# Performance work log

Hardware: AMD Instinct MI355X
Metric: run time of the kernel (lower is better)

## Reference

```python
import jax, jax.numpy as jnp
import numpy as np

B, T = 64, 512
EMBED, HIDDEN, NUM_CLASSES = 512, 1024, 256


def setup_inputs() -> dict:
    key = jax.random.key(0)
    ks = jax.random.split(key, 8)
    x = jax.random.randint(ks[0], (B, T), 0, NUM_CLASSES, dtype=jnp.int32)
    # embedding init uniform(-0.1, 0.1) as in the torch module
    embed = jax.random.uniform(ks[1], (NUM_CLASSES, EMBED), minval=-0.1, maxval=0.1, dtype=jnp.float32)
    s_ih = 1.0 / np.sqrt(HIDDEN)
    W_ih = jax.random.uniform(ks[2], (4 * HIDDEN, EMBED), minval=-s_ih, maxval=s_ih, dtype=jnp.float32)
    W_hh = jax.random.uniform(ks[3], (4 * HIDDEN, HIDDEN), minval=-s_ih, maxval=s_ih, dtype=jnp.float32)
    b_ih = jax.random.uniform(ks[4], (4 * HIDDEN,), minval=-s_ih, maxval=s_ih, dtype=jnp.float32)
    b_hh = jax.random.uniform(ks[5], (4 * HIDDEN,), minval=-s_ih, maxval=s_ih, dtype=jnp.float32)
    s_fc = 1.0 / np.sqrt(HIDDEN)
    fc_W = jax.random.uniform(ks[6], (NUM_CLASSES, HIDDEN), minval=-s_fc, maxval=s_fc, dtype=jnp.float32)
    fc_b = jax.random.uniform(ks[7], (NUM_CLASSES,), minval=-s_fc, maxval=s_fc, dtype=jnp.float32)
    return {"x": x, "embed": embed, "W_ih": W_ih, "W_hh": W_hh,
            "b_ih": b_ih, "b_hh": b_hh, "fc_W": fc_W, "fc_b": fc_b}


def _lstm_forward(x, embed, W_ih, W_hh, b_ih, b_hh, fc_W, fc_b):
    H = W_hh.shape[1]
    x_embed = embed[x]                      # [B, T, E]
    # Precompute input-side gate projections for all timesteps at once.
    gates_x = jnp.einsum('bte,ge->btg', x_embed, W_ih) + (b_ih + b_hh)  # [B, T, 4H]
    gates_x = jnp.transpose(gates_x, (1, 0, 2))  # [T, B, 4H]

    def step(carry, g_x):
        h, c = carry
        gates = g_x + h @ W_hh.T            # [B, 4H]
        i, f, g, o = jnp.split(gates, 4, axis=-1)  # torch gate order: i,f,g,o
        i = jax.nn.sigmoid(i)
        f = jax.nn.sigmoid(f)
        g = jnp.tanh(g)
        o = jax.nn.sigmoid(o)
        c = f * c + i * g
        h = o * jnp.tanh(c)
        return (h, c), h

    Bn = x.shape[0]
    h0 = jnp.zeros((Bn, H), dtype=embed.dtype)
    c0 = jnp.zeros((Bn, H), dtype=embed.dtype)
    _, hs = jax.lax.scan(step, (h0, c0), gates_x)   # hs: [T, B, H]
    hs = jnp.transpose(hs, (1, 0, 2))               # [B, T, H]
    out = jnp.einsum('bth,ch->btc', hs, fc_W) + fc_b  # [B, T, C]
    return out


def reference(x, embed, W_ih, W_hh, b_ih, b_hh, fc_W, fc_b):
    return _lstm_forward(x, embed, W_ih, W_hh, b_ih, b_hh, fc_W, fc_b)
```

## Files before the change

kernel.cpp:

```cpp
#include <hip/hip_runtime.h>
#include <math.h>

#define DEV_INLINE __device__ __forceinline__

static constexpr int Bn = 64;
static constexpr int Tn = 512;
static constexpr int En = 512;
static constexpr int Hn = 1024;
static constexpr int Cn = 256;
static constexpr int Gn = 4 * Hn;

typedef float v4f __attribute__((ext_vector_type(4)));
typedef _Float16 v8h __attribute__((ext_vector_type(8)));

DEV_INLINE float sigmoidf_(float v) { return 1.f / (1.f + __expf(-v)); }

__global__ __launch_bounds__(256) void gemm_tt(
    const float* __restrict__ A, const float* __restrict__ Bm,
    const float* __restrict__ bias1, const float* __restrict__ bias2,
    float* __restrict__ Cm, int M, int N, int K)
{
  constexpr int KC = 32;
  __shared__ float As[KC][68];
  __shared__ float Bs[KC][68];
  const int tid = threadIdx.x;
  const int tx = tid & 15, ty = tid >> 4;
  const int m0 = blockIdx.x * 64, n0 = blockIdx.y * 64;

  float acc[4][4] = {};

  for (int k0 = 0; k0 < K; k0 += KC) {
    __syncthreads();
    #pragma unroll
    for (int j = 0; j < 2; ++j) {
      int f = tid + j * 256;
      int row = f >> 3;
      int c4 = f & 7;
      float4 va = *reinterpret_cast<const float4*>(&A[(size_t)(m0 + row) * K + k0 + c4 * 4]);
      As[c4 * 4 + 0][row] = va.x; As[c4 * 4 + 1][row] = va.y;
      As[c4 * 4 + 2][row] = va.z; As[c4 * 4 + 3][row] = va.w;
      float4 vb = *reinterpret_cast<const float4*>(&Bm[(size_t)(n0 + row) * K + k0 + c4 * 4]);
      Bs[c4 * 4 + 0][row] = vb.x; Bs[c4 * 4 + 1][row] = vb.y;
      Bs[c4 * 4 + 2][row] = vb.z; Bs[c4 * 4 + 3][row] = vb.w;
    }
    __syncthreads();
    #pragma unroll
    for (int k = 0; k < KC; ++k) {
      float4 a4 = *reinterpret_cast<const float4*>(&As[k][ty * 4]);
      float4 b4 = *reinterpret_cast<const float4*>(&Bs[k][tx * 4]);
      float ar[4] = {a4.x, a4.y, a4.z, a4.w};
      float br[4] = {b4.x, b4.y, b4.z, b4.w};
      #pragma unroll
      for (int i = 0; i < 4; ++i)
        #pragma unroll
        for (int j = 0; j < 4; ++j)
          acc[i][j] += ar[i] * br[j];
    }
  }

  #pragma unroll
  for (int j = 0; j < 4; ++j) {
    int n = n0 + tx * 4 + j;
    float bb = bias1[n];
    if (bias2) bb += bias2[n];
    #pragma unroll
    for (int i = 0; i < 4; ++i)
      Cm[(size_t)(m0 + ty * 4 + i) * N + n] = acc[i][j] + bb;
  }
}

__global__ __launch_bounds__(256) void cvt_fcw(
    const float* __restrict__ fcW, _Float16* __restrict__ fcW16)
{
  const int idx = (blockIdx.x * 256 + threadIdx.x) * 8;
  float4 f0 = *(const float4*)(fcW + idx);
  float4 f1 = *(const float4*)(fcW + idx + 4);
  v8h h8;
  h8[0] = (_Float16)f0.x; h8[1] = (_Float16)f0.y;
  h8[2] = (_Float16)f0.z; h8[3] = (_Float16)f0.w;
  h8[4] = (_Float16)f1.x; h8[5] = (_Float16)f1.y;
  h8[6] = (_Float16)f1.z; h8[7] = (_Float16)f1.w;
  *(v8h*)(fcW16 + idx) = h8;
}

__global__ __launch_bounds__(512, 2) void lstm_fused(
    const int* __restrict__ x,
    const float* __restrict__ Whh,
    const float* __restrict__ proj,
    _Float16* __restrict__ hs16,
    int* __restrict__ flags,
    const _Float16* __restrict__ fcW16,
    const float* __restrict__ fcb,
    float* __restrict__ out)
{
  __shared__ __align__(16) char hT[32768];
  __shared__ _Float16 hstage[512];

  const int tid = threadIdx.x;
  const int bid = blockIdx.x;

  const int w = tid >> 6, l = tid & 63;
  const int mrow = l & 15;
  const int kseg = l >> 4;

  const int srcoff = (tid & 15) * 2048 + ((tid >> 4) & 3) * 16 + (tid >> 6) * 64;

  if (bid < 128) {
    const int bg = bid >> 5, hg = bid & 31;
    const int b0 = bg * 16;

    v8h wv[32];
    {
      const float* wr = Whh
        + (size_t)((mrow & 3) * Hn + hg * 32 + w * 4 + (mrow >> 2)) * Hn
        + kseg * 8;
      #pragma unroll
      for (int kk = 0; kk < 32; ++kk) {
        const float* p = wr + kk * 32;
        float4 f0 = *(const float4*)p, f1 = *(const float4*)(p + 4);
        v8h h8;
        h8[0] = (_Float16)f0.x; h8[1] = (_Float16)f0.y;
        h8[2] = (_Float16)f0.z; h8[3] = (_Float16)f0.w;
        h8[4] = (_Float16)f1.x; h8[5] = (_Float16)f1.y;
        h8[6] = (_Float16)f1.z; h8[7] = (_Float16)f1.w;
        wv[kk] = h8;
      }
    }

    const int eb = mrow;
    const int ehc = w * 4 + kseg;
    const int* xp = x + (size_t)(b0 + eb) * Tn;
    float cst = 0.f;

    for (int t = 0; t < Tn; ++t) {
      const int cls = xp[t];
      const float* pb = proj + (size_t)cls * Gn + hg * 32 + ehc;
      float p0 = pb[0], p1 = pb[Hn], p2 = pb[2 * Hn], p3 = pb[3 * Hn];

      if (t > 0) {
        if (tid < 32) {
          const int* fp = flags + ((size_t)(t - 1) * 4 + bg) * 32 + tid;
          int v;
          do {
            asm volatile(
              "global_load_dword %0, %1, off sc0 sc1\n\t"
              "s_waitcnt vmcnt(0)"
              : "=v"(v) : "v"(fp) : "memory");
          } while (v == 0);
        }
        __syncthreads();

        const char* src = (const char*)(hs16 + ((size_t)(t - 1) * Bn + b0) * Hn);
        const char* s0 = src + srcoff;
        v4f r0, r1, r2, r3;
        asm volatile(
          "global_load_dwordx4 %0, %4, off sc0 sc1\n\t"
          "global_load_dwordx4 %1, %5, off sc0 sc1\n\t"
          "global_load_dwordx4 %2, %6, off sc0 sc1\n\t"
          "global_load_dwordx4 %3, %7, off sc0 sc1\n\t"
          "s_waitcnt vmcnt(0)"
          : "=&v"(r0), "=&v"(r1), "=&v"(r2), "=&v"(r3)
          : "v"(s0), "v"(s0 + 512), "v"(s0 + 1024), "v"(s0 + 1536)
          : "memory");
        *(v4f*)(hT + tid * 16 +     0) = r0;
        *(v4f*)(hT + tid * 16 +  8192) = r1;
        *(v4f*)(hT + tid * 16 + 16384) = r2;
        *(v4f*)(hT + tid * 16 + 24576) = r3;
      }
      __syncthreads();

      v4f acc0 = {0.f, 0.f, 0.f, 0.f};
      v4f acc1 = {0.f, 0.f, 0.f, 0.f};
      if (t > 0) {
        #pragma unroll
        for (int kk = 0; kk < 32; kk += 2) {
          v8h a0 = *(const v8h*)(hT + kk * 1024 + l * 16);
          v8h a1 = *(const v8h*)(hT + (kk + 1) * 1024 + l * 16);
          acc0 = __builtin_amdgcn_mfma_f32_16x16x32_f16(wv[kk], a0, acc0, 0, 0, 0);
          acc1 = __builtin_amdgcn_mfma_f32_16x16x32_f16(wv[kk + 1], a1, acc1, 0, 0, 0);
        }
      }

      {
        float g0 = acc0[0] + acc1[0] + p0;
        float g1 = acc0[1] + acc1[1] + p1;
        float g2 = acc0[2] + acc1[2] + p2;
        float g3 = acc0[3] + acc1[3] + p3;
        float ig = sigmoidf_(g0), fg = sigmoidf_(g1);
        float gg = tanhf(g2),     og = sigmoidf_(g3);
        cst = fg * cst + ig * gg;
        hstage[eb * 32 + ehc] = (_Float16)(og * tanhf(cst));
      }
      __syncthreads();

      if (tid < 64) {
        const int b = tid >> 2, part = tid & 3;
        v4f v = *(const v4f*)(hstage + b * 32 + part * 8);
        _Float16* dp = hs16 + ((size_t)t * Bn + b0 + b) * Hn + hg * 32 + part * 8;
        asm volatile(
          "global_store_dwordx4 %0, %1, off sc0 sc1\n\t"
          "s_waitcnt vmcnt(0)"
          :: "v"(dp), "v"(v) : "memory");
        if (tid == 0) {
          int one = 1;
          int* fq = flags + ((size_t)t * 4 + bg) * 32 + hg;
          asm volatile(
            "global_store_dword %0, %1, off sc0 sc1\n\t"
            "s_waitcnt vmcnt(0)"
            :: "v"(fq), "v"(one) : "memory");
        }
      }
    }
  } else {
    const int fid = bid - 128;

    for (int j = 0; j < 16; ++j) {
      const int unit = j * 128 + fid;
      const int t = unit >> 2, bgf = unit & 3;
      const int b0f = bgf * 16;

      if (tid < 32) {
        const int* fp = flags + ((size_t)t * 4 + bgf) * 32 + tid;
        int v;
        for (;;) {
          asm volatile(
            "global_load_dword %0, %1, off sc0 sc1\n\t"
            "s_waitcnt vmcnt(0)"
            : "=v"(v) : "v"(fp) : "memory");
          if (v != 0) break;
          __builtin_amdgcn_s_sleep(16);
        }
      }
      __syncthreads();

      {
        const char* src = (const char*)(hs16 + ((size_t)t * Bn + b0f) * Hn);
        const char* s0 = src + srcoff;
        v4f r0, r1, r2, r3;
        asm volatile(
          "global_load_dwordx4 %0, %4, off sc0 sc1\n\t"
          "global_load_dwordx4 %1, %5, off sc0 sc1\n\t"
          "global_load_dwordx4 %2, %6, off sc0 sc1\n\t"
          "global_load_dwordx4 %3, %7, off sc0 sc1\n\t"
          "s_waitcnt vmcnt(0)"
          : "=&v"(r0), "=&v"(r1), "=&v"(r2), "=&v"(r3)
          : "v"(s0), "v"(s0 + 512), "v"(s0 + 1024), "v"(s0 + 1536)
          : "memory");
        *(v4f*)(hT + tid * 16 +     0) = r0;
        *(v4f*)(hT + tid * 16 +  8192) = r1;
        *(v4f*)(hT + tid * 16 + 16384) = r2;
        *(v4f*)(hT + tid * 16 + 24576) = r3;
      }
      __syncthreads();

      #pragma unroll
      for (int nt = 0; nt < 2; ++nt) {
        const int clsbase = w * 32 + nt * 16;
        v4f acc = {0.f, 0.f, 0.f, 0.f};
        const _Float16* ab = fcW16 + (size_t)(clsbase + mrow) * Hn + kseg * 8;
        #pragma unroll
        for (int kk = 0; kk < 32; ++kk) {
          v8h af = *(const v8h*)(ab + kk * 32);
          v8h bf = *(const v8h*)(hT + kk * 1024 + l * 16);
          acc = __builtin_amdgcn_mfma_f32_16x16x32_f16(af, bf, acc, 0, 0, 0);
        }
        v4f b4 = *(const v4f*)(fcb + clsbase + kseg * 4);
        v4f res = {acc[0] + b4[0], acc[1] + b4[1], acc[2] + b4[2], acc[3] + b4[3]};
        float* op = out + ((size_t)(b0f + mrow) * Tn + t) * Cn + clsbase + kseg * 4;
        *(v4f*)op = res;
      }
    }
  }
}

extern "C" void kernel_launch(void* const* d_in, const int* in_sizes, int n_in,
                              void* d_out, int out_size, void* d_ws, size_t ws_size,
                              hipStream_t stream) {
  const int*   x     = (const int*)  d_in[0];
  const float* embed = (const float*)d_in[1];
  const float* Wih   = (const float*)d_in[2];
  const float* Whh   = (const float*)d_in[3];
  const float* bih   = (const float*)d_in[4];
  const float* bhh   = (const float*)d_in[5];
  const float* fcW   = (const float*)d_in[6];
  const float* fcb   = (const float*)d_in[7];
  float* out = (float*)d_out;

  char* ws = (char*)d_ws;
  const size_t flagBytes = (size_t)Tn * 4 * 32 * 4;
  const size_t projBytes = (size_t)Cn * Gn * sizeof(float);
  const size_t hsBytes   = (size_t)Tn * Bn * Hn * sizeof(_Float16);
  const size_t fw16Bytes = (size_t)Cn * Hn * sizeof(_Float16);
  const size_t need = flagBytes + projBytes + hsBytes + fw16Bytes;
  if (ws_size < need) {
    hipMemsetAsync(d_out, 0, (size_t)out_size * sizeof(float), stream);
    return;
  }
  float*     proj  = (float*)(ws + flagBytes);
  _Float16*  hs16  = (_Float16*)(ws + flagBytes + projBytes);
  _Float16*  fcW16 = (_Float16*)(ws + flagBytes + projBytes + hsBytes);

  hipMemsetAsync(d_ws, 0, flagBytes, stream);

  cvt_fcw<<<128, 256, 0, stream>>>(fcW, fcW16);

  dim3 g1(Cn / 64, Gn / 64);
  gemm_tt<<<g1, 256, 0, stream>>>(embed, Wih, bih, bhh, proj, Cn, Gn, En);

  lstm_fused<<<256, 512, 0, stream>>>(x, Whh, proj, hs16, (int*)d_ws,
                                      fcW16, fcb, out);
}
```

Measured before the change: 1.992 ms.

## Split recurrent step into two half-K phases to overlap flag waits with compute

The recurrent LSTM blocks now wait on the first 16 producer flags, load the first half of h_{t-1}, and run the first half of the MFMA reduction. Meanwhile they wait on the remaining 16 flags and load the second half. This is meant to overlap cross-block synchronisation latency and global loads with matrix work on the serial critical path. The hstage buffer is padded to a stride of 40 to reduce LDS bank conflicts, and the projection-side sleep in the polling loop is lengthened to cut contention. In exchange there are extra __syncthreads per step, including a trailing one.

After: 1.974 ms, median of 2. No clear change (-0.9%).

```diff
diff --git a/kernel.cpp b/kernel.cpp
--- a/kernel.cpp
+++ b/kernel.cpp
@@ -94,7 +94,7 @@
     float* __restrict__ out)
 {
   __shared__ __align__(16) char hT[32768];
-  __shared__ _Float16 hstage[512];
+  __shared__ _Float16 hstage[16 * 40];
 
   const int tid = threadIdx.x;
   const int bid = blockIdx.x;
@@ -137,8 +137,13 @@
       const float* pb = proj + (size_t)cls * Gn + hg * 32 + ehc;
       float p0 = pb[0], p1 = pb[Hn], p2 = pb[2 * Hn], p3 = pb[3 * Hn];
 
+      v4f acc0 = {0.f, 0.f, 0.f, 0.f};
+      v4f acc1 = {0.f, 0.f, 0.f, 0.f};
+
       if (t > 0) {
-        if (tid < 32) {
+        const char* s0 = (const char*)(hs16 + ((size_t)(t - 1) * Bn + b0) * Hn)
+                       + srcoff;
+        if (tid < 16) {
           const int* fp = flags + ((size_t)(t - 1) * 4 + bg) * 32 + tid;
           int v;
           do {
@@ -149,9 +154,108 @@
           } while (v == 0);
         }
         __syncthreads();
-
-        const char* src = (const char*)(hs16 + ((size_t)(t - 1) * Bn + b0) * Hn);
-        const char* s0 = src + srcoff;
+        v4f r0, r1, r2, r3;
+        asm volatile(
+          "global_load_dwordx4 %0, %2, off sc0 sc1\n\t"
+          "global_load_dwordx4 %1, %3, off sc0 sc1"
+          : "=&v"(r0), "=&v"(r1)
+          : "v"(s0), "v"(s0 + 512) : "memory");
+        if (tid >= 16 && tid < 32) {
+          const int* fp = flags + ((size_t)(t - 1) * 4 + bg) * 32 + tid;
+          int v;
+          do {
+            asm volatile(
+              "global_load_dword %0, %1, off sc0 sc1\n\t"
+              "s_waitcnt vmcnt(0)"
+              : "=v"(v) : "v"(fp) : "memory");
+          } while (v == 0);
+        }
+        __syncthreads();
+        asm volatile(
+          "global_load_dwordx4 %0, %2, off sc0 sc1\n\t"
+          "global_load_dwordx4 %1, %3, off sc0 sc1"
+          : "=&v"(r2), "=&v"(r3)
+          : "v"(s0 + 1024), "v"(s0 + 1536) : "memory");
+        asm volatile("s_waitcnt vmcnt(2)" ::: "memory");
+        *(v4f*)(hT + tid * 16 +    0) = r0;
+        *(v4f*)(hT + tid * 16 + 8192) = r1;
+        __syncthreads();
+        #pragma unroll
+        for (int kk = 0; kk < 16; kk += 2) {
+          v8h a0 = *(const v8h*)(hT + kk * 1024 + l * 16);
+          v8h a1 = *(const v8h*)(hT + (kk + 1) * 1024 + l * 16);
+          acc0 = __builtin_amdgcn_mfma_f32_16x16x32_f16(wv[kk], a0, acc0, 0, 0, 0);
+          acc1 = __builtin_amdgcn_mfma_f32_16x16x32_f16(wv[kk + 1], a1, acc1, 0, 0, 0);
+        }
+        asm volatile("s_waitcnt vmcnt(0)" ::: "memory");
+        *(v4f*)(hT + tid * 16 + 16384) = r2;
+        *(v4f*)(hT + tid * 16 + 24576) = r3;
+        __syncthreads();
+        #pragma unroll
+        for (int kk = 16; kk < 32; kk += 2) {
+          v8h a0 = *(const v8h*)(hT + kk * 1024 + l * 16);
+          v8h a1 = *(const v8h*)(hT + (kk + 1) * 1024 + l * 16);
+          acc0 = __builtin_amdgcn_mfma_f32_16x16x32_f16(wv[kk], a0, acc0, 0, 0, 0);
+          acc1 = __builtin_amdgcn_mfma_f32_16x16x32_f16(wv[kk + 1], a1, acc1, 0, 0, 0);
+        }
+      }
+
+      {
+        float g0 = acc0[0] + acc1[0] + p0;
+        float g1 = acc0[1] + acc1[1] + p1;
+        float g2 = acc0[2] + acc1[2] + p2;
+        float g3 = acc0[3] + acc1[3] + p3;
+        float ig = sigmoidf_(g0), fg = sigmoidf_(g1);
+        float gg = tanhf(g2),     og = sigmoidf_(g3);
+        cst = fg * cst + ig * gg;
+        hstage[eb * 40 + ehc] = (_Float16)(og * tanhf(cst));
+      }
+      __syncthreads();
+
+      if (tid < 64) {
+        const int b = tid >> 2, part = tid & 3;
+        v4f v = *(const v4f*)(hstage + b * 40 + part * 8);
+        _Float16* dp = hs16 + ((size_t)t * Bn + b0 + b) * Hn + hg * 32 + part * 8;
+        asm volatile(
+          "global_store_dwordx4 %0, %1, off sc0 sc1\n\t"
+          "s_waitcnt vmcnt(0)"
+          :: "v"(dp), "v"(v) : "memory");
+        if (tid == 0) {
+          int one = 1;
+          int* fq = flags + ((size_t)t * 4 + bg) * 32 + hg;
+          asm volatile(
+            "global_store_dword %0, %1, off sc0 sc1\n\t"
+            "s_waitcnt vmcnt(0)"
+            :: "v"(fq), "v"(one) : "memory");
+        }
+      }
+      __syncthreads();
+    }
+  } else {
+    const int fid = bid - 128;
+
+    for (int j = 0; j < 16; ++j) {
+      const int unit = j * 128 + fid;
+      const int t = unit >> 2, bgf = unit & 3;
+      const int b0f = bgf * 16;
+
+      if (tid < 32) {
+        const int* fp = flags + ((size_t)t * 4 + bgf) * 32 + tid;
+        int v;
+        for (;;) {
+          asm volatile(
+            "global_load_dword %0, %1, off sc0 sc1\n\t"
+            "s_waitcnt vmcnt(0)"
+            : "=v"(v) : "v"(fp) : "memory");
+          if (v != 0) break;
+          __builtin_amdgcn_s_sleep(64);
+        }
+      }
+      __syncthreads();
+
+      {
+        const char* s0 = (const char*)(hs16 + ((size_t)t * Bn + b0f) * Hn)
+                       + srcoff;
         v4f r0, r1, r2, r3;
         asm volatile(
           "global_load_dwordx4 %0, %4, off sc0 sc1\n\t"
@@ -169,90 +273,6 @@
       }
       __syncthreads();
 
-      v4f acc0 = {0.f, 0.f, 0.f, 0.f};
-      v4f acc1 = {0.f, 0.f, 0.f, 0.f};
-      if (t > 0) {
-        #pragma unroll
-        for (int kk = 0; kk < 32; kk += 2) {
-          v8h a0 = *(const v8h*)(hT + kk * 1024 + l * 16);
-          v8h a1 = *(const v8h*)(hT + (kk + 1) * 1024 + l * 16);
-          acc0 = __builtin_amdgcn_mfma_f32_16x16x32_f16(wv[kk], a0, acc0, 0, 0, 0);
-          acc1 = __builtin_amdgcn_mfma_f32_16x16x32_f16(wv[kk + 1], a1, acc1, 0, 0, 0);
-        }
-      }
-
-      {
-        float g0 = acc0[0] + acc1[0] + p0;
-        float g1 = acc0[1] + acc1[1] + p1;
-        float g2 = acc0[2] + acc1[2] + p2;
-        float g3 = acc0[3] + acc1[3] + p3;
-        float ig = sigmoidf_(g0), fg = sigmoidf_(g1);
-        float gg = tanhf(g2),     og = sigmoidf_(g3);
-        cst = fg * cst + ig * gg;
-        hstage[eb * 32 + ehc] = (_Float16)(og * tanhf(cst));
-      }
-      __syncthreads();
-
-      if (tid < 64) {
-        const int b = tid >> 2, part = tid & 3;
-        v4f v = *(const v4f*)(hstage + b * 32 + part * 8);
-        _Float16* dp = hs16 + ((size_t)t * Bn + b0 + b) * Hn + hg * 32 + part * 8;
-        asm volatile(
-          "global_store_dwordx4 %0, %1, off sc0 sc1\n\t"
-          "s_waitcnt vmcnt(0)"
-          :: "v"(dp), "v"(v) : "memory");
-        if (tid == 0) {
-          int one = 1;
-          int* fq = flags + ((size_t)t * 4 + bg) * 32 + hg;
-          asm volatile(
-            "global_store_dword %0, %1, off sc0 sc1\n\t"
-            "s_waitcnt vmcnt(0)"
-            :: "v"(fq), "v"(one) : "memory");
-        }
-      }
-    }
-  } else {
-    const int fid = bid - 128;
-
-    for (int j = 0; j < 16; ++j) {
-      const int unit = j * 128 + fid;
-      const int t = unit >> 2, bgf = unit & 3;
-      const int b0f = bgf * 16;
-
-      if (tid < 32) {
-        const int* fp = flags + ((size_t)t * 4 + bgf) * 32 + tid;
-        int v;
-        for (;;) {
-          asm volatile(
-            "global_load_dword %0, %1, off sc0 sc1\n\t"
-            "s_waitcnt vmcnt(0)"
-            : "=v"(v) : "v"(fp) : "memory");
-          if (v != 0) break;
-          __builtin_amdgcn_s_sleep(16);
-        }
-      }
-      __syncthreads();
-
-      {
-        const char* src = (const char*)(hs16 + ((size_t)t * Bn + b0f) * Hn);
-        const char* s0 = src + srcoff;
-        v4f r0, r1, r2, r3;
-        asm volatile(
-          "global_load_dwordx4 %0, %4, off sc0 sc1\n\t"
-          "global_load_dwordx4 %1, %5, off sc0 sc1\n\t"
-          "global_load_dwordx4 %2, %6, off sc0 sc1\n\t"
-          "global_load_dwordx4 %3, %7, off sc0 sc1\n\t"
-          "s_waitcnt vmcnt(0)"
-          : "=&v"(r0), "=&v"(r1), "=&v"(r2), "=&v"(r3)
-          : "v"(s0), "v"(s0 + 512), "v"(s0 + 1024), "v"(s0 + 1536)
-          : "memory");
-        *(v4f*)(hT + tid * 16 +     0) = r0;
-        *(v4f*)(hT + tid * 16 +  8192) = r1;
-        *(v4f*)(hT + tid * 16 + 16384) = r2;
-        *(v4f*)(hT + tid * 16 + 24576) = r3;
-      }
-      __syncthreads();
-
       #pragma unroll
       for (int nt = 0; nt < 2; ++nt) {
         const int clsbase = w * 32 + nt * 16;
```
